# Optimization experiments

Measured on AMD Instinct MI355X. Metric: run time of the kernel, lower is better.

## Reference

```python
import jax, jax.numpy as jnp
import numpy as np

N_NODES = 30000
N_EDGES = 480000
B_PAIRS = 4096


def _lin(key, fan_in, fan_out):
    k1, k2 = jax.random.split(key)
    s = 1.0 / np.sqrt(fan_in)
    W = jax.random.uniform(k1, (fan_in, fan_out), minval=-s, maxval=s, dtype=jnp.float32)
    b = jax.random.uniform(k2, (fan_out,), minval=-s, maxval=s, dtype=jnp.float32)
    return W, b


def setup_inputs() -> dict:
    key = jax.random.key(0)
    ks = jax.random.split(key, 20)
    inp = {}
    inp["cid"] = jax.random.normal(ks[0], (N_NODES, 881), dtype=jnp.float32)
    inp["link_edge"] = jax.random.randint(ks[1], (2, N_EDGES), 0, N_NODES, dtype=jnp.int64)
    inp["i1"] = jax.random.randint(ks[2], (B_PAIRS,), 0, N_NODES, dtype=jnp.int64)
    inp["i2"] = jax.random.randint(ks[3], (B_PAIRS,), 0, N_NODES, dtype=jnp.int64)
    inp["soft_thr"] = jnp.array(0.01, jnp.float32)
    inp["bb_fc2_W"], inp["bb_fc2_b"] = _lin(ks[4], 881, 881)
    inp["bb_fc3_W"], inp["bb_fc3_b"] = _lin(ks[5], 881, 256)
    inp["gcn1_W"], inp["gcn1_b"] = _lin(ks[6], 256, 256)
    inp["gcn2_W"], inp["gcn2_b"] = _lin(ks[7], 256, 256)
    inp["gcn3_W"], inp["gcn3_b"] = _lin(ks[8], 256, 256)
    inp["gcn4_W"], inp["gcn4_b"] = _lin(ks[9], 256, 128)
    inp["gcn5_W"], inp["gcn5_b"] = _lin(ks[10], 128, 128)
    inp["fc1_W"], inp["fc1_b"] = _lin(ks[11], 256, 1024)
    inp["fc2_W"], inp["fc2_b"] = _lin(ks[12], 1024, 256)
    inp["fc3_W"], inp["fc3_b"] = _lin(ks[13], 256, 64)
    inp["out_W"], inp["out_b"] = _lin(ks[14], 64, 2)
    return inp


def _forward(cid, link_edge, i1, i2, soft_thr,
             bb_fc2_W, bb_fc2_b, bb_fc3_W, bb_fc3_b,
             gcn1_W, gcn1_b, gcn2_W, gcn2_b, gcn3_W, gcn3_b,
             gcn4_W, gcn4_b, gcn5_W, gcn5_b,
             fc1_W, fc1_b, fc2_W, fc2_b, fc3_W, fc3_b, out_W, out_b):
    N = cid.shape[0]
    # --- BasicBlock1 (eval mode, dropout off everywhere) ---
    x = jax.nn.relu(cid @ bb_fc2_W + bb_fc2_b)
    x = jnp.sign(x) * jax.nn.relu(jnp.abs(x) - soft_thr)  # soft threshold
    x = jax.nn.relu(x @ bb_fc3_W + bb_fc3_b)              # [N, 256]

    # --- GCN normalization (PyG GCNConv: add self-loops, sym norm) ---
    loop = jnp.arange(N, dtype=link_edge.dtype)
    src = jnp.concatenate([link_edge[0], loop])
    dst = jnp.concatenate([link_edge[1], loop])
    deg = jax.ops.segment_sum(jnp.ones_like(dst, dtype=jnp.float32), dst, num_segments=N)
    dinv = jnp.where(deg > 0, jax.lax.rsqrt(deg), 0.0)
    enorm = (dinv[src] * dinv[dst])[:, None]  # [E+N, 1]

    def gcn(h, W, b):
        h = h @ W                                            # [N, F_out]
        msg = h[src] * enorm                                 # gather + scale
        return jax.ops.segment_sum(msg, dst, num_segments=N) + b

    h = jax.nn.elu(gcn(x, gcn1_W, gcn1_b))
    h = jax.nn.elu(gcn(h, gcn2_W, gcn2_b))
    h = jax.nn.elu(gcn(h, gcn3_W, gcn3_b))
    h = jax.nn.elu(gcn(h, gcn4_W, gcn4_b))
    h = jax.nn.elu(gcn(h, gcn5_W, gcn5_b))                   # [N, 128]

    # --- pair readout ---
    xc = jnp.concatenate([h[i1], h[i2]], axis=1)             # [B, 256]
    norm = jnp.maximum(jnp.linalg.norm(xc, axis=1, keepdims=True), 1e-12)
    xc = xc / norm                                           # F.normalize(p=2, dim=1)
    xc = jax.nn.relu(xc @ fc1_W + fc1_b)
    xc = jax.nn.relu(xc @ fc2_W + fc2_b)
    xc = jax.nn.relu(xc @ fc3_W + fc3_b)
    return xc @ out_W + out_b                                # [B, 2]


def reference(cid, link_edge, i1, i2, soft_thr,
              bb_fc2_W, bb_fc2_b, bb_fc3_W, bb_fc3_b,
              gcn1_W, gcn1_b, gcn2_W, gcn2_b, gcn3_W, gcn3_b,
              gcn4_W, gcn4_b, gcn5_W, gcn5_b,
              fc1_W, fc1_b, fc2_W, fc2_b, fc3_W, fc3_b, out_W, out_b):
    return _forward(cid, link_edge, i1, i2, soft_thr,
                    bb_fc2_W, bb_fc2_b, bb_fc3_W, bb_fc3_b,
                    gcn1_W, gcn1_b, gcn2_W, gcn2_b, gcn3_W, gcn3_b,
                    gcn4_W, gcn4_b, gcn5_W, gcn5_b,
                    fc1_W, fc1_b, fc2_W, fc2_b, fc3_W, fc3_b, out_W, out_b)
```

## Files before the change

### kernel.cpp

```cpp
#include <hip/hip_runtime.h>
#include <hip/hip_bf16.h>
#include <math.h>


#define NNODES 30000
#define NEDGES 480000
#define NPAIRS 4096

typedef __attribute__((ext_vector_type(8))) short short8;
typedef __attribute__((ext_vector_type(2))) short short2v;
typedef __attribute__((ext_vector_type(4))) short short4v;
typedef __attribute__((ext_vector_type(4))) float f32x4;
typedef __attribute__((ext_vector_type(2))) float f32x2;
typedef unsigned short u16;

__device__ __forceinline__ u16 f2bf(float x) {
    union { float f; unsigned u; } v; v.f = x;
    unsigned u = v.u;
    return (u16)((u + 0x7FFFu + ((u >> 16) & 1u)) >> 16);
}
__device__ __forceinline__ float bf2f(u16 h) {
    union { float f; unsigned u; } v; v.u = ((unsigned)h) << 16;
    return v.f;
}


__global__ void k_count(const int* __restrict__ dst, unsigned* __restrict__ cnt, int E) {
    int e = blockIdx.x * blockDim.x + threadIdx.x;
    if (e < E) atomicAdd(&cnt[dst[e]], 1u);
}

__global__ void k_dinv(const unsigned* __restrict__ cnt, float* __restrict__ dinv, int N) {
    int n = blockIdx.x * blockDim.x + threadIdx.x;
    if (n < N) {
        float deg = (float)(cnt[n] + 1u);
        dinv[n] = 1.0f / sqrtf(deg);
    }
}

__global__ void k_scan(const unsigned* __restrict__ cnt, unsigned* __restrict__ rowptr, int N) {
    __shared__ unsigned buf[1024];
    __shared__ unsigned carry_s;
    const int tid = threadIdx.x;
    if (tid == 0) { carry_s = 0; rowptr[0] = 0; }
    __syncthreads();
    for (int base = 0; base < N; base += 1024) {
        int i = base + tid;
        unsigned v = (i < N) ? cnt[i] : 0u;
        buf[tid] = v;
        __syncthreads();
        for (int off = 1; off < 1024; off <<= 1) {
            unsigned t = (tid >= off) ? buf[tid - off] : 0u;
            __syncthreads();
            buf[tid] += t;
            __syncthreads();
        }
        unsigned c = carry_s;
        if (i < N) rowptr[i + 1] = c + buf[tid];
        __syncthreads();
        if (tid == 1023) carry_s = c + buf[1023];
        __syncthreads();
    }
}

__global__ void k_fill(const int* __restrict__ src, const int* __restrict__ dst,
                       const unsigned* __restrict__ rowptr, unsigned* __restrict__ cursor,
                       int* __restrict__ colsrc, int E) {
    int e = blockIdx.x * blockDim.x + threadIdx.x;
    if (e < E) {
        int d = dst[e];
        unsigned p = atomicAdd(&cursor[d], 1u);
        colsrc[rowptr[d] + p] = src[e];
    }
}


__global__ void k_wconv(const float* __restrict__ W, u16* __restrict__ Th,
                        u16* __restrict__ Tl, int K, int N, int Kp, int Np) {
    int idx = blockIdx.x * blockDim.x + threadIdx.x;
    if (idx >= Np * Kp) return;
    int n = idx / Kp, k = idx - n * Kp;
    float v = (n < N && k < K) ? W[(size_t)k * N + n] : 0.f;
    u16 h = f2bf(v);
    Th[idx] = h;
    Tl[idx] = f2bf(v - bf2f(h));
}


#define LDSW 40

template <int ASRC, int EPI, int OUTM>
__global__ __launch_bounds__(256) void k_mgemm(
    const float* __restrict__ Af, int ldAf, int Ktrue,
    const u16* __restrict__ Ahi, const u16* __restrict__ Alo, int ldA,
    const u16* __restrict__ Bhi, const u16* __restrict__ Blo,
    const float* __restrict__ bias, const float* __restrict__ thrp,
    float* __restrict__ Cf, u16* __restrict__ Chi, u16* __restrict__ Clo,
    int ldC, int M, int Ntrue, int K) {
    __shared__ alignas(16) u16 Ah[128 * LDSW];
    __shared__ alignas(16) u16 Al[128 * LDSW];
    __shared__ alignas(16) u16 Bh[128 * LDSW];
    __shared__ alignas(16) u16 Bl[128 * LDSW];
    const int t = threadIdx.x;
    const int lane = t & 63, w = t >> 6;
    const int wr = w >> 1, wc = w & 1;
    const int r16 = lane & 15, kg = lane >> 4;
    const int bm = blockIdx.x * 128, bn = blockIdx.y * 128;
    const int sr = t & 127, cb = (t >> 7) << 4;
    f32x4 acc[4][4] = {};

    float aF[16];
    short8 aP[4], bP[4];

    auto LOAD = [&](int k0) {
        if (ASRC == 0) {
            const int gm = bm + sr;
            const int gmc = gm < M ? gm : M - 1;
            const float* ap = Af + (size_t)gmc * ldAf + k0 + cb;
            const int nv = Ktrue - (k0 + cb);
#pragma unroll
            for (int j = 0; j < 16; ++j) {
                int jc = j < nv ? j : nv - 1;
                aF[j] = ap[jc];
            }
        } else {
            const u16* ah = Ahi + (size_t)(bm + sr) * ldA + k0 + cb;
            const u16* al = Alo + (size_t)(bm + sr) * ldA + k0 + cb;
            aP[0] = *(const short8*)ah;  aP[1] = *(const short8*)(ah + 8);
            aP[2] = *(const short8*)al;  aP[3] = *(const short8*)(al + 8);
        }
        const u16* bh = Bhi + (size_t)(bn + sr) * K + k0 + cb;
        const u16* bl = Blo + (size_t)(bn + sr) * K + k0 + cb;
        bP[0] = *(const short8*)bh;  bP[1] = *(const short8*)(bh + 8);
        bP[2] = *(const short8*)bl;  bP[3] = *(const short8*)(bl + 8);
    };

    auto WRITE = [&](int k0) {
        const int wa = sr * LDSW + cb;
        if (ASRC == 0) {
            const int nv = Ktrue - (k0 + cb);
            short8 h0, h1, l0, l1;
#pragma unroll
            for (int j = 0; j < 8; ++j) {
                float v = (j < nv) ? aF[j] : 0.f;
                u16 hh = f2bf(v);
                h0[j] = (short)hh;
                l0[j] = (short)f2bf(v - bf2f(hh));
            }
#pragma unroll
            for (int j = 0; j < 8; ++j) {
                float v = (j + 8 < nv) ? aF[j + 8] : 0.f;
                u16 hh = f2bf(v);
                h1[j] = (short)hh;
                l1[j] = (short)f2bf(v - bf2f(hh));
            }
            *(short8*)&Ah[wa] = h0;  *(short8*)&Ah[wa + 8] = h1;
            *(short8*)&Al[wa] = l0;  *(short8*)&Al[wa + 8] = l1;
        } else {
            *(short8*)&Ah[wa] = aP[0];  *(short8*)&Ah[wa + 8] = aP[1];
            *(short8*)&Al[wa] = aP[2];  *(short8*)&Al[wa + 8] = aP[3];
        }
        *(short8*)&Bh[wa] = bP[0];  *(short8*)&Bh[wa + 8] = bP[1];
        *(short8*)&Bl[wa] = bP[2];  *(short8*)&Bl[wa + 8] = bP[3];
    };

    LOAD(0);
    for (int k0 = 0; k0 < K; k0 += 32) {
        WRITE(k0);
        __syncthreads();
        if (k0 + 32 < K) LOAD(k0 + 32);
        short8 fa_h[4], fa_l[4];
#pragma unroll
        for (int mi = 0; mi < 4; ++mi) {
            int off = (wr * 64 + mi * 16 + r16) * LDSW + kg * 8;
            fa_h[mi] = *(const short8*)&Ah[off];
            fa_l[mi] = *(const short8*)&Al[off];
        }
#pragma unroll
        for (int ni = 0; ni < 4; ++ni) {
            int off = (wc * 64 + ni * 16 + r16) * LDSW + kg * 8;
            short8 fb_h = *(const short8*)&Bh[off];
            short8 fb_l = *(const short8*)&Bl[off];
#pragma unroll
            for (int mi = 0; mi < 4; ++mi) {
                acc[mi][ni] = __builtin_amdgcn_mfma_f32_16x16x32_bf16(fa_h[mi], fb_h, acc[mi][ni], 0, 0, 0);
                acc[mi][ni] = __builtin_amdgcn_mfma_f32_16x16x32_bf16(fa_l[mi], fb_h, acc[mi][ni], 0, 0, 0);
                acc[mi][ni] = __builtin_amdgcn_mfma_f32_16x16x32_bf16(fa_h[mi], fb_l, acc[mi][ni], 0, 0, 0);
            }
        }
        __syncthreads();
    }

    const float thr = (EPI == 2) ? *thrp : 0.f;
#pragma unroll
    for (int mi = 0; mi < 4; ++mi) {
#pragma unroll
        for (int ni = 0; ni < 4; ++ni) {
            const int n = bn + wc * 64 + ni * 16 + r16;
#pragma unroll
            for (int i = 0; i < 4; ++i) {
                const int m = bm + wr * 64 + mi * 16 + kg * 4 + i;
                if (m >= M) continue;
                float z = acc[mi][ni][i];
                if (EPI >= 1) {
                    z += (n < Ntrue) ? bias[n] : 0.f;
                    z = (EPI == 1) ? fmaxf(z, 0.f) : fmaxf(z - thr, 0.f);
                }
                if (OUTM == 0) {
                    if (n < Ntrue) Cf[(size_t)m * ldC + n] = z;
                } else {
                    if (n < ldC) {
                        if (n >= Ntrue) z = 0.f;
                        u16 h = f2bf(z);
                        size_t o = (size_t)m * ldC + n;
                        Chi[o] = h;
                        Clo[o] = f2bf(z - bf2f(h));
                    }
                }
            }
        }
    }
}


template <int FV, int WB>
__global__ __launch_bounds__(256) void k_agg(
    const float* __restrict__ hW, const float* __restrict__ dinv,
    const unsigned* __restrict__ rowptr, const int* __restrict__ colsrc,
    const float* __restrict__ bias, float* __restrict__ outf,
    u16* __restrict__ oh, u16* __restrict__ ol, int N) {
    const int wave = threadIdx.x >> 6;
    const int lane = threadIdx.x & 63;
    const int n = blockIdx.x * 4 + wave;
    if (n >= N) return;
    const int F = FV * 64;
    const int fb = lane * FV;
    const float dn = dinv[n];
    float acc[FV];
    if (FV == 4) {
        const f32x4 v = *(const f32x4*)(hW + (size_t)n * F + fb);
#pragma unroll
        for (int j = 0; j < FV; ++j) acc[j] = dn * v[j];
    } else {
        const f32x2 v = *(const f32x2*)(hW + (size_t)n * F + fb);
#pragma unroll
        for (int j = 0; j < FV; ++j) acc[j] = dn * v[j];
    }
    const unsigned beg = rowptr[n], end = rowptr[n + 1];
    for (unsigned idx = beg; idx < end; ++idx) {
        int s = colsrc[idx];
        float wsc = dinv[s];
        if (FV == 4) {
            const f32x4 v = *(const f32x4*)(hW + (size_t)s * F + fb);
#pragma unroll
            for (int j = 0; j < FV; ++j) acc[j] += wsc * v[j];
        } else {
            const f32x2 v = *(const f32x2*)(hW + (size_t)s * F + fb);
#pragma unroll
            for (int j = 0; j < FV; ++j) acc[j] += wsc * v[j];
        }
    }
    float z[FV];
#pragma unroll
    for (int j = 0; j < FV; ++j) {
        float zz = dn * acc[j] + bias[fb + j];
        z[j] = (zz > 0.f) ? zz : expm1f(zz);
    }
    if (WB) {
        if (FV == 4) {
            short4v hv, lv;
#pragma unroll
            for (int j = 0; j < 4; ++j) {
                u16 h = f2bf(z[j]);
                hv[j] = (short)h;
                lv[j] = (short)f2bf(z[j] - bf2f(h));
            }
            *(short4v*)(oh + (size_t)n * F + fb) = hv;
            *(short4v*)(ol + (size_t)n * F + fb) = lv;
        } else {
            short2v hv, lv;
#pragma unroll
            for (int j = 0; j < 2; ++j) {
                u16 h = f2bf(z[j]);
                hv[j] = (short)h;
                lv[j] = (short)f2bf(z[j] - bf2f(h));
            }
            *(short2v*)(oh + (size_t)n * F + fb) = hv;
            *(short2v*)(ol + (size_t)n * F + fb) = lv;
        }
    } else {
        if (FV == 4) {
            f32x4 v;
#pragma unroll
            for (int j = 0; j < 4; ++j) v[j] = z[j];
            *(f32x4*)(outf + (size_t)n * F + fb) = v;
        } else {
            f32x2 v;
#pragma unroll
            for (int j = 0; j < 2; ++j) v[j] = z[j];
            *(f32x2*)(outf + (size_t)n * F + fb) = v;
        }
    }
}


__global__ __launch_bounds__(256) void k_pairs(
    const float* __restrict__ h, const int* __restrict__ i1, const int* __restrict__ i2,
    u16* __restrict__ xh, u16* __restrict__ xl, int B) {
    const int wave = threadIdx.x >> 6;
    const int lane = threadIdx.x & 63;
    const int p = blockIdx.x * 4 + wave;
    if (p >= B) return;
    const int a = i1[p], b = i2[p];
    float v0 = h[(size_t)a * 128 + lane];
    float v1 = h[(size_t)a * 128 + 64 + lane];
    float v2 = h[(size_t)b * 128 + lane];
    float v3 = h[(size_t)b * 128 + 64 + lane];
    float ss = v0 * v0 + v1 * v1 + v2 * v2 + v3 * v3;
#pragma unroll
    for (int o = 32; o > 0; o >>= 1) ss += __shfl_xor(ss, o, 64);
    float scale = 1.0f / fmaxf(sqrtf(ss), 1e-12f);
    size_t o = (size_t)p * 256;
    float vv[4] = {v0 * scale, v1 * scale, v2 * scale, v3 * scale};
#pragma unroll
    for (int j = 0; j < 4; ++j) {
        u16 hh = f2bf(vv[j]);
        xh[o + j * 64 + lane] = hh;
        xl[o + j * 64 + lane] = f2bf(vv[j] - bf2f(hh));
    }
}

__global__ __launch_bounds__(256) void k_out(
    const float* __restrict__ x, const float* __restrict__ W, const float* __restrict__ b,
    float* __restrict__ out, int B) {
    const int wave = threadIdx.x >> 6;
    const int lane = threadIdx.x & 63;
    const int p = blockIdx.x * 4 + wave;
    if (p >= B) return;
    float v = x[(size_t)p * 64 + lane];
    float s0 = v * W[lane * 2 + 0];
    float s1 = v * W[lane * 2 + 1];
#pragma unroll
    for (int o = 32; o > 0; o >>= 1) {
        s0 += __shfl_xor(s0, o, 64);
        s1 += __shfl_xor(s1, o, 64);
    }
    if (lane == 0) {
        out[p * 2 + 0] = s0 + b[0];
        out[p * 2 + 1] = s1 + b[1];
    }
}


extern "C" void kernel_launch(void* const* d_in, const int* in_sizes, int n_in,
                              void* d_out, int out_size, void* d_ws, size_t ws_size,
                              hipStream_t stream) {
    const float* cid = (const float*)d_in[0];
    const int* le   = (const int*)d_in[1];
    const int* i1   = (const int*)d_in[2];
    const int* i2   = (const int*)d_in[3];
    const float* thr = (const float*)d_in[4];
    const float* W2 = (const float*)d_in[5];  const float* b2 = (const float*)d_in[6];
    const float* W3 = (const float*)d_in[7];  const float* b3 = (const float*)d_in[8];
    const float* gW[5] = {(const float*)d_in[9],  (const float*)d_in[11], (const float*)d_in[13],
                          (const float*)d_in[15], (const float*)d_in[17]};
    const float* gB[5] = {(const float*)d_in[10], (const float*)d_in[12], (const float*)d_in[14],
                          (const float*)d_in[16], (const float*)d_in[18]};
    const float* fc1W = (const float*)d_in[19]; const float* fc1b = (const float*)d_in[20];
    const float* fc2W = (const float*)d_in[21]; const float* fc2b = (const float*)d_in[22];
    const float* fc3W = (const float*)d_in[23]; const float* fc3b = (const float*)d_in[24];
    const float* oW   = (const float*)d_in[25]; const float* ob   = (const float*)d_in[26];

    const int N = NNODES, E = NEDGES, B = NPAIRS;
    char* ws = (char*)d_ws;

    unsigned* cnt    = (unsigned*)(ws + 0);
    unsigned* cursor = (unsigned*)(ws + 120064);
    unsigned* rowptr = (unsigned*)(ws + 240128);
    int*      colsrc = (int*)     (ws + 360192);
    float*    dinv   = (float*)   (ws + 2280192);

    u16* W2th = (u16*)(ws + 2400256);  u16* W2tl = (u16*)(ws + 4005888);
    u16* W3th = (u16*)(ws + 5611520);  u16* W3tl = (u16*)(ws + 6070272);
    u16* g1h  = (u16*)(ws + 6529024);  u16* g1l  = (u16*)(ws + 6660096);
    u16* g2h  = (u16*)(ws + 6791168);  u16* g2l  = (u16*)(ws + 6922240);
    u16* g3h  = (u16*)(ws + 7053312);  u16* g3l  = (u16*)(ws + 7184384);
    u16* g4h  = (u16*)(ws + 7315456);  u16* g4l  = (u16*)(ws + 7380992);
    u16* g5h  = (u16*)(ws + 7446528);  u16* g5l  = (u16*)(ws + 7479296);
    u16* f1h  = (u16*)(ws + 7512064);  u16* f1l  = (u16*)(ws + 8036352);
    u16* f2h  = (u16*)(ws + 8560640);  u16* f2l  = (u16*)(ws + 9084928);
    u16* f3h  = (u16*)(ws + 9609216);  u16* f3l  = (u16*)(ws + 9674752);

    u16* x2h = (u16*)(ws + 9740288);
    u16* x2l = (u16*)(ws + 25141248);
    const size_t X1 = 40542208;
    u16* x1h = (u16*)(ws + X1);
    u16* x1l = (u16*)(ws + X1 + 53903360);
    float* hW   = (float*)(ws + X1);
    u16*   hAh  = (u16*)  (ws + X1 + 30720000);
    u16*   hAl  = (u16*)  (ws + X1 + 46120960);
    float* hfin = (float*)(ws + X1 + 61521920);
    u16*   xch  = (u16*)  (ws + X1 + 76881920);
    u16*   xcl  = (u16*)  (ws + X1 + 78979072);
    u16*   t1h  = (u16*)  (ws + X1 + 81076224);
    u16*   t1l  = (u16*)  (ws + X1 + 89464832);
    u16*   t2h  = (u16*)  (ws + X1 + 97853440);
    u16*   t2l  = (u16*)  (ws + X1 + 99950592);
    float* t3   = (float*)(ws + X1 + 102047744);

    hipMemsetAsync(cnt, 0, N * sizeof(unsigned), stream);
    hipMemsetAsync(cursor, 0, N * sizeof(unsigned), stream);
    k_count<<<(E + 255) / 256, 256, 0, stream>>>(le + E, cnt, E);
    k_dinv<<<(N + 255) / 256, 256, 0, stream>>>(cnt, dinv, N);
    k_scan<<<1, 1024, 0, stream>>>(cnt, rowptr, N);
    k_fill<<<(E + 255) / 256, 256, 0, stream>>>(le, le + E, rowptr, cursor, colsrc, E);

    k_wconv<<<3136, 256, 0, stream>>>(W2, W2th, W2tl, 881, 881, 896, 896);
    k_wconv<<<896, 256, 0, stream>>>(W3, W3th, W3tl, 881, 256, 896, 256);
    k_wconv<<<256, 256, 0, stream>>>(gW[0], g1h, g1l, 256, 256, 256, 256);
    k_wconv<<<256, 256, 0, stream>>>(gW[1], g2h, g2l, 256, 256, 256, 256);
    k_wconv<<<256, 256, 0, stream>>>(gW[2], g3h, g3l, 256, 256, 256, 256);
    k_wconv<<<128, 256, 0, stream>>>(gW[3], g4h, g4l, 256, 128, 256, 128);
    k_wconv<<<64, 256, 0, stream>>>(gW[4], g5h, g5l, 128, 128, 128, 128);
    k_wconv<<<1024, 256, 0, stream>>>(fc1W, f1h, f1l, 256, 1024, 256, 1024);
    k_wconv<<<1024, 256, 0, stream>>>(fc2W, f2h, f2l, 1024, 256, 1024, 256);
    k_wconv<<<128, 256, 0, stream>>>(fc3W, f3h, f3l, 256, 64, 256, 128);

    const int MB = (N + 127) / 128;

    k_mgemm<0, 2, 1><<<dim3(MB, 7), 256, 0, stream>>>(
        cid, 881, 881, nullptr, nullptr, 0, W2th, W2tl, b2, thr,
        nullptr, x1h, x1l, 896, N, 881, 896);
    k_mgemm<1, 1, 1><<<dim3(MB, 2), 256, 0, stream>>>(
        nullptr, 0, 0, x1h, x1l, 896, W3th, W3tl, b3, nullptr,
        nullptr, x2h, x2l, 256, N, 256, 896);

    const u16* wh[5] = {g1h, g2h, g3h, g4h, g5h};
    const u16* wl[5] = {g1l, g2l, g3l, g4l, g5l};
    const int fin[5]  = {256, 256, 256, 256, 128};
    const int fout[5] = {256, 256, 256, 128, 128};
    u16* curh = x2h;  u16* curl = x2l;
    for (int l = 0; l < 5; ++l) {
        k_mgemm<1, 0, 0><<<dim3(MB, fout[l] / 128), 256, 0, stream>>>(
            nullptr, 0, 0, curh, curl, fin[l], wh[l], wl[l], nullptr, nullptr,
            hW, nullptr, nullptr, fout[l], N, fout[l], fin[l]);
        if (l == 4) {
            k_agg<2, 0><<<(N + 3) / 4, 256, 0, stream>>>(hW, dinv, rowptr, colsrc, gB[l],
                                                         hfin, nullptr, nullptr, N);
        } else if (fout[l] == 256) {
            u16* oh = (l & 1) ? x2h : hAh;
            u16* ol = (l & 1) ? x2l : hAl;
            k_agg<4, 1><<<(N + 3) / 4, 256, 0, stream>>>(hW, dinv, rowptr, colsrc, gB[l],
                                                         nullptr, oh, ol, N);
            curh = oh; curl = ol;
        } else {
            k_agg<2, 1><<<(N + 3) / 4, 256, 0, stream>>>(hW, dinv, rowptr, colsrc, gB[l],
                                                         nullptr, x2h, x2l, N);
            curh = x2h; curl = x2l;
        }
    }

    k_pairs<<<(B + 3) / 4, 256, 0, stream>>>(hfin, i1, i2, xch, xcl, B);
    k_mgemm<1, 1, 1><<<dim3(32, 8), 256, 0, stream>>>(
        nullptr, 0, 0, xch, xcl, 256, f1h, f1l, fc1b, nullptr,
        nullptr, t1h, t1l, 1024, B, 1024, 256);
    k_mgemm<1, 1, 1><<<dim3(32, 2), 256, 0, stream>>>(
        nullptr, 0, 0, t1h, t1l, 1024, f2h, f2l, fc2b, nullptr,
        nullptr, t2h, t2l, 256, B, 256, 1024);
    k_mgemm<1, 1, 0><<<dim3(32, 1), 256, 0, stream>>>(
        nullptr, 0, 0, t2h, t2l, 256, f3h, f3l, fc3b, nullptr,
        t3, nullptr, nullptr, 64, B, 64, 256);
    k_out<<<(B + 3) / 4, 256, 0, stream>>>(t3, oW, ob, (float*)d_out, B);
}
```

Baseline: 1.363 ms.

## Use direct global-to-LDS loads in GEMM, XCD-aware tile mapping, prescaled aggregation

The split-bf16 GEMM now moves A/B tiles straight from global memory into unpadded LDS with global_load_lds, replacing register staging and its software prefetch. A 1D grid is remapped so consecutive tiles stay on the same XCD for L2 reuse. GCN linear outputs are prescaled by dinv in the GEMM epilogue, so the aggregation kernel drops its per-edge dinv gather and is unrolled by two edges. Risks are LDS bank conflicts from removing the padding, and losing load/compute overlap since prefetch is gone.

Result: no change. 1.360 ms (-0.2%).

```diff
diff --git a/kernel.cpp b/kernel.cpp
--- a/kernel.cpp
+++ b/kernel.cpp
@@ -8,8 +8,8 @@
 #define NPAIRS 4096
 
 typedef __attribute__((ext_vector_type(8))) short short8;
+typedef __attribute__((ext_vector_type(4))) short short4v;
 typedef __attribute__((ext_vector_type(2))) short short2v;
-typedef __attribute__((ext_vector_type(4))) short short4v;
 typedef __attribute__((ext_vector_type(4))) float f32x4;
 typedef __attribute__((ext_vector_type(2))) float f32x2;
 typedef unsigned short u16;
@@ -22,6 +22,12 @@
 __device__ __forceinline__ float bf2f(u16 h) {
     union { float f; unsigned u; } v; v.u = ((unsigned)h) << 16;
     return v.f;
+}
+
+__device__ __forceinline__ void gll16(const u16* g, u16* l) {
+    __builtin_amdgcn_global_load_lds(
+        (const __attribute__((address_space(1))) unsigned int*)g,
+        (__attribute__((address_space(3))) unsigned int*)l, 16, 0, 0);
 }
 
 
@@ -87,120 +93,97 @@
 }
 
 
-#define LDSW 40
-
 template <int ASRC, int EPI, int OUTM>
 __global__ __launch_bounds__(256) void k_mgemm(
     const float* __restrict__ Af, int ldAf, int Ktrue,
     const u16* __restrict__ Ahi, const u16* __restrict__ Alo, int ldA,
-    const u16* __restrict__ Bhi, const u16* __restrict__ Blo,
+    const u16* __restrict__ Bhi, const u16* __restrict__ Blo, int ldB,
     const float* __restrict__ bias, const float* __restrict__ thrp,
+    const float* __restrict__ rowscale,
     float* __restrict__ Cf, u16* __restrict__ Chi, u16* __restrict__ Clo,
-    int ldC, int M, int Ntrue, int K) {
-    __shared__ alignas(16) u16 Ah[128 * LDSW];
-    __shared__ alignas(16) u16 Al[128 * LDSW];
-    __shared__ alignas(16) u16 Bh[128 * LDSW];
-    __shared__ alignas(16) u16 Bl[128 * LDSW];
+    int ldC, int M, int Ntrue, int K, int gy) {
+    __shared__ alignas(16) u16 Ah[128 * 32];
+    __shared__ alignas(16) u16 Al[128 * 32];
+    __shared__ alignas(16) u16 Bh[128 * 32];
+    __shared__ alignas(16) u16 Bl[128 * 32];
     const int t = threadIdx.x;
     const int lane = t & 63, w = t >> 6;
     const int wr = w >> 1, wc = w & 1;
     const int r16 = lane & 15, kg = lane >> 4;
-    const int bm = blockIdx.x * 128, bn = blockIdx.y * 128;
-    const int sr = t & 127, cb = (t >> 7) << 4;
+    const int nwg = gridDim.x;
+    const int q = nwg >> 3, r = nwg & 7;
+    const int xcd = blockIdx.x & 7, pos = blockIdx.x >> 3;
+    const int wg = (xcd < r ? xcd * (q + 1) : r * (q + 1) + (xcd - r) * q) + pos;
+    const int bx = wg / gy, by = wg - bx * gy;
+    const int bm = bx * 128, bn = by * 128;
+    const int srow = (w << 5) + (lane >> 2);
+    const int k8 = (lane & 3) << 3;
+    const int lb = w << 11;
     f32x4 acc[4][4] = {};
 
-    float aF[16];
-    short8 aP[4], bP[4];
-
-    auto LOAD = [&](int k0) {
+    for (int k0 = 0; k0 < K; k0 += 32) {
         if (ASRC == 0) {
-            const int gm = bm + sr;
-            const int gmc = gm < M ? gm : M - 1;
-            const float* ap = Af + (size_t)gmc * ldAf + k0 + cb;
-            const int nv = Ktrue - (k0 + cb);
-#pragma unroll
-            for (int j = 0; j < 16; ++j) {
-                int jc = j < nv ? j : nv - 1;
-                aF[j] = ap[jc];
+            const int arow = t >> 1, kq = (t & 1) << 4;
+            int gm = bm + arow; if (gm >= M) gm = M - 1;
+            const size_t base = (size_t)gm * ldAf;
+#pragma unroll
+            for (int jj = 0; jj < 2; ++jj) {
+                short8 hv, lv;
+#pragma unroll
+                for (int j = 0; j < 8; ++j) {
+                    const int k = k0 + kq + jj * 8 + j;
+                    float v = (k < Ktrue) ? Af[base + k] : 0.f;
+                    u16 hh = f2bf(v);
+                    hv[j] = (short)hh;
+                    lv[j] = (short)f2bf(v - bf2f(hh));
+                }
+                *(short8*)&Ah[arow * 32 + kq + jj * 8] = hv;
+                *(short8*)&Al[arow * 32 + kq + jj * 8] = lv;
             }
         } else {
-            const u16* ah = Ahi + (size_t)(bm + sr) * ldA + k0 + cb;
-            const u16* al = Alo + (size_t)(bm + sr) * ldA + k0 + cb;
-            aP[0] = *(const short8*)ah;  aP[1] = *(const short8*)(ah + 8);
-            aP[2] = *(const short8*)al;  aP[3] = *(const short8*)(al + 8);
-        }
-        const u16* bh = Bhi + (size_t)(bn + sr) * K + k0 + cb;
-        const u16* bl = Blo + (size_t)(bn + sr) * K + k0 + cb;
-        bP[0] = *(const short8*)bh;  bP[1] = *(const short8*)(bh + 8);
-        bP[2] = *(const short8*)bl;  bP[3] = *(const short8*)(bl + 8);
-    };
-
-    auto WRITE = [&](int k0) {
-        const int wa = sr * LDSW + cb;
-        if (ASRC == 0) {
-            const int nv = Ktrue - (k0 + cb);
-            short8 h0, h1, l0, l1;
-#pragma unroll
-            for (int j = 0; j < 8; ++j) {
-                float v = (j < nv) ? aF[j] : 0.f;
-                u16 hh = f2bf(v);
-                h0[j] = (short)hh;
-                l0[j] = (short)f2bf(v - bf2f(hh));
+            gll16(Ahi + (size_t)(bm + srow) * ldA + k0 + k8, (u16*)((char*)Ah + lb));
+            gll16(Ahi + (size_t)(bm + srow + 16) * ldA + k0 + k8, (u16*)((char*)Ah + lb + 1024));
+            gll16(Alo + (size_t)(bm + srow) * ldA + k0 + k8, (u16*)((char*)Al + lb));
+            gll16(Alo + (size_t)(bm + srow + 16) * ldA + k0 + k8, (u16*)((char*)Al + lb + 1024));
+        }
+        gll16(Bhi + (size_t)(bn + srow) * ldB + k0 + k8, (u16*)((char*)Bh + lb));
+        gll16(Bhi + (size_t)(bn + srow + 16) * ldB + k0 + k8, (u16*)((char*)Bh + lb + 1024));
+        gll16(Blo + (size_t)(bn + srow) * ldB + k0 + k8, (u16*)((char*)Bl + lb));
+        gll16(Blo + (size_t)(bn + srow + 16) * ldB + k0 + k8, (u16*)((char*)Bl + lb + 1024));
+        __syncthreads();
+        short8 fah[4], fal[4];
+#pragma unroll
+        for (int mi = 0; mi < 4; ++mi) {
+            const int off = (wr * 64 + mi * 16 + r16) * 32 + kg * 8;
+            fah[mi] = *(const short8*)&Ah[off];
+            fal[mi] = *(const short8*)&Al[off];
+        }
+#pragma unroll
+        for (int ni = 0; ni < 4; ++ni) {
+            const int off = (wc * 64 + ni * 16 + r16) * 32 + kg * 8;
+            const short8 fbh = *(const short8*)&Bh[off];
+            const short8 fbl = *(const short8*)&Bl[off];
+#pragma unroll
+            for (int mi = 0; mi < 4; ++mi) {
+                acc[mi][ni] = __builtin_amdgcn_mfma_f32_16x16x32_bf16(fah[mi], fbh, acc[mi][ni], 0, 0, 0);
+                acc[mi][ni] = __builtin_amdgcn_mfma_f32_16x16x32_bf16(fal[mi], fbh, acc[mi][ni], 0, 0, 0);
+                acc[mi][ni] = __builtin_amdgcn_mfma_f32_16x16x32_bf16(fah[mi], fbl, acc[mi][ni], 0, 0, 0);
             }
-#pragma unroll
-            for (int j = 0; j < 8; ++j) {
-                float v = (j + 8 < nv) ? aF[j + 8] : 0.f;
-                u16 hh = f2bf(v);
-                h1[j] = (short)hh;
-                l1[j] = (short)f2bf(v - bf2f(hh));
-            }
-            *(short8*)&Ah[wa] = h0;  *(short8*)&Ah[wa + 8] = h1;
-            *(short8*)&Al[wa] = l0;  *(short8*)&Al[wa + 8] = l1;
-        } else {
-            *(short8*)&Ah[wa] = aP[0];  *(short8*)&Ah[wa + 8] = aP[1];
-            *(short8*)&Al[wa] = aP[2];  *(short8*)&Al[wa + 8] = aP[3];
-        }
-        *(short8*)&Bh[wa] = bP[0];  *(short8*)&Bh[wa + 8] = bP[1];
-        *(short8*)&Bl[wa] = bP[2];  *(short8*)&Bl[wa + 8] = bP[3];
-    };
-
-    LOAD(0);
-    for (int k0 = 0; k0 < K; k0 += 32) {
-        WRITE(k0);
+        }
         __syncthreads();
-        if (k0 + 32 < K) LOAD(k0 + 32);
-        short8 fa_h[4], fa_l[4];
-#pragma unroll
-        for (int mi = 0; mi < 4; ++mi) {
-            int off = (wr * 64 + mi * 16 + r16) * LDSW + kg * 8;
-            fa_h[mi] = *(const short8*)&Ah[off];
-            fa_l[mi] = *(const short8*)&Al[off];
-        }
-#pragma unroll
-        for (int ni = 0; ni < 4; ++ni) {
-            int off = (wc * 64 + ni * 16 + r16) * LDSW + kg * 8;
-            short8 fb_h = *(const short8*)&Bh[off];
-            short8 fb_l = *(const short8*)&Bl[off];
-#pragma unroll
-            for (int mi = 0; mi < 4; ++mi) {
-                acc[mi][ni] = __builtin_amdgcn_mfma_f32_16x16x32_bf16(fa_h[mi], fb_h, acc[mi][ni], 0, 0, 0);
-                acc[mi][ni] = __builtin_amdgcn_mfma_f32_16x16x32_bf16(fa_l[mi], fb_h, acc[mi][ni], 0, 0, 0);
-                acc[mi][ni] = __builtin_amdgcn_mfma_f32_16x16x32_bf16(fa_h[mi], fb_l, acc[mi][ni], 0, 0, 0);
-            }
-        }
-        __syncthreads();
     }
 
     const float thr = (EPI == 2) ? *thrp : 0.f;
 #pragma unroll
     for (int mi = 0; mi < 4; ++mi) {
 #pragma unroll
-        for (int ni = 0; ni < 4; ++ni) {
-            const int n = bn + wc * 64 + ni * 16 + r16;
-#pragma unroll
-            for (int i = 0; i < 4; ++i) {
-                const int m = bm + wr * 64 + mi * 16 + kg * 4 + i;
-                if (m >= M) continue;
+        for (int i = 0; i < 4; ++i) {
+            const int m = bm + wr * 64 + mi * 16 + kg * 4 + i;
+            if (m >= M) continue;
+            const float rs = (OUTM == 2) ? rowscale[m] : 1.f;
+#pragma unroll
+            for (int ni = 0; ni < 4; ++ni) {
+                const int n = bn + wc * 64 + ni * 16 + r16;
                 float z = acc[mi][ni][i];
                 if (EPI >= 1) {
                     z += (n < Ntrue) ? bias[n] : 0.f;
@@ -208,6 +191,8 @@
                 }
                 if (OUTM == 0) {
                     if (n < Ntrue) Cf[(size_t)m * ldC + n] = z;
+                } else if (OUTM == 2) {
+                    if (n < Ntrue) Cf[(size_t)m * ldC + n] = z * rs;
                 } else {
                     if (n < ldC) {
                         if (n >= Ntrue) z = 0.f;
@@ -225,7 +210,7 @@
 
 template <int FV, int WB>
 __global__ __launch_bounds__(256) void k_agg(
-    const float* __restrict__ hW, const float* __restrict__ dinv,
+    const float* __restrict__ hWs, const float* __restrict__ dinv,
     const unsigned* __restrict__ rowptr, const int* __restrict__ colsrc,
     const float* __restrict__ bias, float* __restrict__ outf,
     u16* __restrict__ oh, u16* __restrict__ ol, int N) {
@@ -235,31 +220,45 @@
     if (n >= N) return;
     const int F = FV * 64;
     const int fb = lane * FV;
-    const float dn = dinv[n];
     float acc[FV];
     if (FV == 4) {
-        const f32x4 v = *(const f32x4*)(hW + (size_t)n * F + fb);
-#pragma unroll
-        for (int j = 0; j < FV; ++j) acc[j] = dn * v[j];
+        const f32x4 v = *(const f32x4*)(hWs + (size_t)n * F + fb);
+#pragma unroll
+        for (int j = 0; j < FV; ++j) acc[j] = v[j];
     } else {
-        const f32x2 v = *(const f32x2*)(hW + (size_t)n * F + fb);
-#pragma unroll
-        for (int j = 0; j < FV; ++j) acc[j] = dn * v[j];
-    }
-    const unsigned beg = rowptr[n], end = rowptr[n + 1];
-    for (unsigned idx = beg; idx < end; ++idx) {
-        int s = colsrc[idx];
-        float wsc = dinv[s];
+        const f32x2 v = *(const f32x2*)(hWs + (size_t)n * F + fb);
+#pragma unroll
+        for (int j = 0; j < FV; ++j) acc[j] = v[j];
+    }
+    unsigned idx = rowptr[n];
+    const unsigned end = rowptr[n + 1];
+    for (; idx + 2 <= end; idx += 2) {
+        int s0 = colsrc[idx], s1 = colsrc[idx + 1];
         if (FV == 4) {
-            const f32x4 v = *(const f32x4*)(hW + (size_t)s * F + fb);
-#pragma unroll
-            for (int j = 0; j < FV; ++j) acc[j] += wsc * v[j];
-        } else {
-            const f32x2 v = *(const f32x2*)(hW + (size_t)s * F + fb);
-#pragma unroll
-            for (int j = 0; j < FV; ++j) acc[j] += wsc * v[j];
-        }
-    }
+            const f32x4 v0 = *(const f32x4*)(hWs + (size_t)s0 * F + fb);
+            const f32x4 v1 = *(const f32x4*)(hWs + (size_t)s1 * F + fb);
+#pragma unroll
+            for (int j = 0; j < FV; ++j) acc[j] += v0[j] + v1[j];
+        } else {
+            const f32x2 v0 = *(const f32x2*)(hWs + (size_t)s0 * F + fb);
+            const f32x2 v1 = *(const f32x2*)(hWs + (size_t)s1 * F + fb);
+#pragma unroll
+            for (int j = 0; j < FV; ++j) acc[j] += v0[j] + v1[j];
+        }
+    }
+    if (idx < end) {
+        int s0 = colsrc[idx];
+        if (FV == 4) {
+            const f32x4 v0 = *(const f32x4*)(hWs + (size_t)s0 * F + fb);
+#pragma unroll
+            for (int j = 0; j < FV; ++j) acc[j] += v0[j];
+        } else {
+            const f32x2 v0 = *(const f32x2*)(hWs + (size_t)s0 * F + fb);
+#pragma unroll
+            for (int j = 0; j < FV; ++j) acc[j] += v0[j];
+        }
+    }
+    const float dn = dinv[n];
     float z[FV];
 #pragma unroll
     for (int j = 0; j < FV; ++j) {
@@ -396,17 +395,17 @@
     const size_t X1 = 40542208;
     u16* x1h = (u16*)(ws + X1);
     u16* x1l = (u16*)(ws + X1 + 53903360);
-    float* hW   = (float*)(ws + X1);
-    u16*   hAh  = (u16*)  (ws + X1 + 30720000);
-    u16*   hAl  = (u16*)  (ws + X1 + 46120960);
-    float* hfin = (float*)(ws + X1 + 61521920);
-    u16*   xch  = (u16*)  (ws + X1 + 76881920);
-    u16*   xcl  = (u16*)  (ws + X1 + 78979072);
-    u16*   t1h  = (u16*)  (ws + X1 + 81076224);
-    u16*   t1l  = (u16*)  (ws + X1 + 89464832);
-    u16*   t2h  = (u16*)  (ws + X1 + 97853440);
-    u16*   t2l  = (u16*)  (ws + X1 + 99950592);
-    float* t3   = (float*)(ws + X1 + 102047744);
+    float* hWs  = (float*)(ws + X1);
+    u16*   hAh  = (u16*)  (ws + X1 + 30801920);
+    u16*   hAl  = (u16*)  (ws + X1 + 46202880);
+    float* hfin = (float*)(ws + X1 + 61603840);
+    u16*   xch  = (u16*)  (ws + X1 + 76963840);
+    u16*   xcl  = (u16*)  (ws + X1 + 79060992);
+    u16*   t1h  = (u16*)  (ws + X1 + 81158144);
+    u16*   t1l  = (u16*)  (ws + X1 + 89546752);
+    u16*   t2h  = (u16*)  (ws + X1 + 97935360);
+    u16*   t2l  = (u16*)  (ws + X1 + 100032512);
+    float* t3   = (float*)(ws + X1 + 102129664);
 
     hipMemsetAsync(cnt, 0, N * sizeof(unsigned), stream);
     hipMemsetAsync(cursor, 0, N * sizeof(unsigned), stream);
@@ -428,12 +427,12 @@
 
     const int MB = (N + 127) / 128;
 
-    k_mgemm<0, 2, 1><<<dim3(MB, 7), 256, 0, stream>>>(
-        cid, 881, 881, nullptr, nullptr, 0, W2th, W2tl, b2, thr,
-        nullptr, x1h, x1l, 896, N, 881, 896);
-    k_mgemm<1, 1, 1><<<dim3(MB, 2), 256, 0, stream>>>(
-        nullptr, 0, 0, x1h, x1l, 896, W3th, W3tl, b3, nullptr,
-        nullptr, x2h, x2l, 256, N, 256, 896);
+    k_mgemm<0, 2, 1><<<MB * 7, 256, 0, stream>>>(
+        cid, 881, 881, nullptr, nullptr, 0, W2th, W2tl, 896, b2, thr, nullptr,
+        nullptr, x1h, x1l, 896, N, 881, 896, 7);
+    k_mgemm<1, 1, 1><<<MB * 2, 256, 0, stream>>>(
+        nullptr, 0, 0, x1h, x1l, 896, W3th, W3tl, 896, b3, nullptr, nullptr,
+        nullptr, x2h, x2l, 256, N, 256, 896, 2);
 
     const u16* wh[5] = {g1h, g2h, g3h, g4h, g5h};
     const u16* wl[5] = {g1l, g2l, g3l, g4l, g5l};
@@ -441,34 +440,35 @@
     const int fout[5] = {256, 256, 256, 128, 128};
     u16* curh = x2h;  u16* curl = x2l;
     for (int l = 0; l < 5; ++l) {
-        k_mgemm<1, 0, 0><<<dim3(MB, fout[l] / 128), 256, 0, stream>>>(
-            nullptr, 0, 0, curh, curl, fin[l], wh[l], wl[l], nullptr, nullptr,
-            hW, nullptr, nullptr, fout[l], N, fout[l], fin[l]);
+        const int gy = fout[l] / 128;
+        k_mgemm<1, 0, 2><<<MB * gy, 256, 0, stream>>>(
+            nullptr, 0, 0, curh, curl, fin[l], wh[l], wl[l], fin[l], nullptr, nullptr, dinv,
+            hWs, nullptr, nullptr, fout[l], N, fout[l], fin[l], gy);
         if (l == 4) {
-            k_agg<2, 0><<<(N + 3) / 4, 256, 0, stream>>>(hW, dinv, rowptr, colsrc, gB[l],
+            k_agg<2, 0><<<(N + 3) / 4, 256, 0, stream>>>(hWs, dinv, rowptr, colsrc, gB[l],
                                                          hfin, nullptr, nullptr, N);
         } else if (fout[l] == 256) {
             u16* oh = (l & 1) ? x2h : hAh;
             u16* ol = (l & 1) ? x2l : hAl;
-            k_agg<4, 1><<<(N + 3) / 4, 256, 0, stream>>>(hW, dinv, rowptr, colsrc, gB[l],
+            k_agg<4, 1><<<(N + 3) / 4, 256, 0, stream>>>(hWs, dinv, rowptr, colsrc, gB[l],
                                                          nullptr, oh, ol, N);
             curh = oh; curl = ol;
         } else {
-            k_agg<2, 1><<<(N + 3) / 4, 256, 0, stream>>>(hW, dinv, rowptr, colsrc, gB[l],
+            k_agg<2, 1><<<(N + 3) / 4, 256, 0, stream>>>(hWs, dinv, rowptr, colsrc, gB[l],
                                                          nullptr, x2h, x2l, N);
             curh = x2h; curl = x2l;
         }
     }
 
     k_pairs<<<(B + 3) / 4, 256, 0, stream>>>(hfin, i1, i2, xch, xcl, B);
-    k_mgemm<1, 1, 1><<<dim3(32, 8), 256, 0, stream>>>(
-        nullptr, 0, 0, xch, xcl, 256, f1h, f1l, fc1b, nullptr,
-        nullptr, t1h, t1l, 1024, B, 1024, 256);
-    k_mgemm<1, 1, 1><<<dim3(32, 2), 256, 0, stream>>>(
-        nullptr, 0, 0, t1h, t1l, 1024, f2h, f2l, fc2b, nullptr,
-        nullptr, t2h, t2l, 256, B, 256, 1024);
-    k_mgemm<1, 1, 0><<<dim3(32, 1), 256, 0, stream>>>(
-        nullptr, 0, 0, t2h, t2l, 256, f3h, f3l, fc3b, nullptr,
-        t3, nullptr, nullptr, 64, B, 64, 256);
+    k_mgemm<1, 1, 1><<<32 * 8, 256, 0, stream>>>(
+        nullptr, 0, 0, xch, xcl, 256, f1h, f1l, 256, fc1b, nullptr, nullptr,
+        nullptr, t1h, t1l, 1024, B, 1024, 256, 8);
+    k_mgemm<1, 1, 1><<<32 * 2, 256, 0, stream>>>(
+        nullptr, 0, 0, t1h, t1l, 1024, f2h, f2l, 1024, fc2b, nullptr, nullptr,
+        nullptr, t2h, t2l, 256, B, 256, 1024, 2);
+    k_mgemm<1, 1, 0><<<32 * 1, 256, 0, stream>>>(
+        nullptr, 0, 0, t2h, t2l, 256, f3h, f3l, 256, fc3b, nullptr, nullptr,
+        t3, nullptr, nullptr, 64, B, 64, 256, 1);
     k_out<<<(B + 3) / 4, 256, 0, stream>>>(t3, oW, ob, (float*)d_out, B);
 }
```
